# Kernel tuning notes

Measured on AMD Instinct MI355X. Metric: run time of the kernel, lower is better.

Reference implementation:

```python
import jax, jax.numpy as jnp
import numpy as np

S = 3136        # tokens (56x56 patch grid, single image segment -> full attention)
H = 16          # num_heads
D = 80          # head_dim (= head_dim_ori = PADDING_HEAD_DIM)
HID = H * D     # 1280
SCALE = 1.0 / float(np.sqrt(D))  # qkScale = 1/sqrt(head_dim_ori)


def _rope_tables(s, d, base=10000.0):
    # rotate_half style: cos/sin of shape [s, d], duplicated over the two halves
    half = d // 2
    inv_freq = 1.0 / (base ** (np.arange(0, half, dtype=np.float32) / half))
    freqs = np.outer(np.arange(s, dtype=np.float32), inv_freq)  # [s, d/2]
    emb = np.concatenate([freqs, freqs], axis=-1)               # [s, d]
    return jnp.asarray(np.cos(emb)), jnp.asarray(np.sin(emb))


def setup_inputs() -> dict:
    key = jax.random.key(0)
    ks = jax.random.split(key, 6)
    cos, sin = _rope_tables(S, D)
    return {
        "hidden_states": jax.random.normal(ks[0], (S, HID), jnp.float32),
        "x_norm": jax.random.normal(ks[1], (S, HID), jnp.float32),
        "qkv_w": jax.random.normal(ks[2], (3 * HID, HID), jnp.float32) * 0.02,
        "qkv_b": jax.random.normal(ks[3], (3 * HID,), jnp.float32) * 0.02,
        "proj_w": jax.random.normal(ks[4], (HID, HID), jnp.float32) * 0.02,
        "proj_b": jax.random.normal(ks[5], (HID,), jnp.float32) * 0.02,
        "cos": cos,
        "sin": sin,
    }


def _rotate_half(x):
    x1, x2 = jnp.split(x, 2, axis=-1)
    return jnp.concatenate([-x2, x1], axis=-1)


def reference(hidden_states, x_norm, qkv_w, qkv_b, proj_w, proj_b, cos, sin):
    # fused QKV linear (transposeB=True) + split into q,k,v along last dim
    qkv = x_norm @ qkv_w.T + qkv_b                      # [S, 3*HID]
    q, k, v = jnp.split(qkv, 3, axis=-1)                # each [S, HID]
    q = q.reshape(S, H, D)
    k = k.reshape(S, H, D)
    v = v.reshape(S, H, D)
    # inline RoPE on q and k (rotate_half over full head_dim)
    c = cos[:, None, :]; s = sin[:, None, :]           # [S,1,D]
    q = q * c + _rotate_half(q) * s
    k = k * c + _rotate_half(k) * s
    # full self-attention (PA_ENCODER, single segment = seq_len S)
    scores = jnp.einsum('shd,thd->hst', q, k) * SCALE   # [H,S,S]
    probs = jax.nn.softmax(scores, axis=-1)
    attn = jnp.einsum('hst,thd->shd', probs, v)         # [S,H,D]
    attn = attn.reshape(S, HID)
    # output projection + residual add
    out = attn @ proj_w.T + proj_b
    return hidden_states + out
```

## Files before the change

### kernel.cpp

```cpp
#include <hip/hip_runtime.h>
#include <hip/hip_bf16.h>

#define S_   3136
#define H_   16
#define D_   80
#define DP_  96
#define HID_ 1280

typedef short  bf16x8 __attribute__((ext_vector_type(8)));
typedef short  bf16x4 __attribute__((ext_vector_type(4)));
typedef float  f32x4  __attribute__((ext_vector_type(4)));

__device__ __forceinline__ float b2f(unsigned short u) {
    union { unsigned int i; float f; } c;
    c.i = ((unsigned int)u) << 16;
    return c.f;
}
__device__ __forceinline__ unsigned short f2b(float f) {
    union { unsigned int i; float f; } c;
    c.f = f;
    unsigned int x = c.i;
    unsigned int lsb = (x >> 16) & 1u;
    x += 0x7fffu + lsb;
    return (unsigned short)(x >> 16);
}

#define N4_X 1003520
#define N4_Q 1228800
#define N4_P 409600

__global__ __launch_bounds__(256)
void cast3_kernel(const float* __restrict__ x0, unsigned short* __restrict__ y0,
                  const float* __restrict__ x1, unsigned short* __restrict__ y1,
                  const float* __restrict__ x2, unsigned short* __restrict__ y2)
{
    int i = blockIdx.x * 256 + threadIdx.x;
    const float* src; unsigned short* dst;
    if (i < N4_X)               { src = x0; dst = y0; }
    else if (i < N4_X + N4_Q)   { src = x1; dst = y1; i -= N4_X; }
    else if (i < N4_X + N4_Q + N4_P) { src = x2; dst = y2; i -= N4_X + N4_Q; }
    else return;
    float4 v = ((const float4*)src)[i];
    ushort4 o;
    o.x = f2b(v.x); o.y = f2b(v.y); o.z = f2b(v.z); o.w = f2b(v.w);
    ((ushort4*)dst)[i] = o;
}

#define ASTR 40

__global__ __launch_bounds__(256)
void qkv_mfma_kernel(const unsigned short* __restrict__ Ab,
                     const unsigned short* __restrict__ Wb,
                     const float* __restrict__ bias,
                     unsigned short* __restrict__ qo, unsigned short* __restrict__ ko,
                     unsigned short* __restrict__ vtb)
{
    __shared__ __align__(16) short As[2][128][ASTR];
    __shared__ __align__(16) short Bs[2][128][ASTR];
    int m0 = blockIdx.x * 128;
    int n0 = blockIdx.y * 128;
    int t = threadIdx.x;
    int wave = t >> 6, lane = t & 63, lq = lane & 15, quad = lane >> 4;
    int wr = wave >> 1, wc = wave & 1;

    int r0  = t >> 2;
    int r1  = r0 + 64;
    int kc0 = (t & 3) << 3;
    const unsigned short* pa0 = Ab + (size_t)min(m0 + r0, S_ - 1) * HID_ + kc0;
    const unsigned short* pa1 = Ab + (size_t)min(m0 + r1, S_ - 1) * HID_ + kc0;
    const unsigned short* pb0 = Wb + (size_t)(n0 + r0) * HID_ + kc0;
    const unsigned short* pb1 = Wb + (size_t)(n0 + r1) * HID_ + kc0;

    const bf16x8* afp[2][4]; const bf16x8* bfp[2][4];
    #pragma unroll
    for (int s = 0; s < 2; ++s)
        #pragma unroll
        for (int i = 0; i < 4; ++i) {
            afp[s][i] = (const bf16x8*)&As[s][wr * 64 + i * 16 + lq][quad * 8];
            bfp[s][i] = (const bf16x8*)&Bs[s][wc * 64 + i * 16 + lq][quad * 8];
        }

    f32x4 acc[4][4];
    #pragma unroll
    for (int i = 0; i < 4; ++i)
        #pragma unroll
        for (int j = 0; j < 4; ++j) acc[i][j] = (f32x4){0.f, 0.f, 0.f, 0.f};

    bf16x8 va[2][2], vb[2][2];
    #pragma unroll
    for (int s = 0; s < 2; ++s) {
        va[s][0] = *(const bf16x8*)(pa0 + s * 32);
        va[s][1] = *(const bf16x8*)(pa1 + s * 32);
        vb[s][0] = *(const bf16x8*)(pb0 + s * 32);
        vb[s][1] = *(const bf16x8*)(pb1 + s * 32);
    }

    for (int kt = 0; kt < HID_; kt += 64) {
        __syncthreads();
        #pragma unroll
        for (int s = 0; s < 2; ++s) {
            *(bf16x8*)&As[s][r0][kc0] = va[s][0];
            *(bf16x8*)&As[s][r1][kc0] = va[s][1];
            *(bf16x8*)&Bs[s][r0][kc0] = vb[s][0];
            *(bf16x8*)&Bs[s][r1][kc0] = vb[s][1];
        }
        __syncthreads();
        if (kt + 64 < HID_) {
            #pragma unroll
            for (int s = 0; s < 2; ++s) {
                va[s][0] = *(const bf16x8*)(pa0 + kt + 64 + s * 32);
                va[s][1] = *(const bf16x8*)(pa1 + kt + 64 + s * 32);
                vb[s][0] = *(const bf16x8*)(pb0 + kt + 64 + s * 32);
                vb[s][1] = *(const bf16x8*)(pb1 + kt + 64 + s * 32);
            }
        }
        #pragma unroll
        for (int s = 0; s < 2; ++s) {
            bf16x8 af[4], bfr[4];
            #pragma unroll
            for (int i = 0; i < 4; ++i) af[i]  = *afp[s][i];
            #pragma unroll
            for (int j = 0; j < 4; ++j) bfr[j] = *bfp[s][j];
            #pragma unroll
            for (int i = 0; i < 4; ++i)
                #pragma unroll
                for (int j = 0; j < 4; ++j)
                    acc[i][j] = __builtin_amdgcn_mfma_f32_16x16x32_bf16(af[i], bfr[j], acc[i][j], 0, 0, 0);
        }
    }

    #pragma unroll
    for (int i = 0; i < 4; ++i)
        #pragma unroll
        for (int j = 0; j < 4; ++j)
            #pragma unroll
            for (int reg = 0; reg < 4; ++reg) {
                int row = m0 + wr * 64 + i * 16 + quad * 4 + reg;
                if (row >= S_) continue;
                int col = n0 + wc * 64 + j * 16 + lq;
                float val = acc[i][j][reg] + bias[col];
                int which = col / HID_;
                int rem   = col - which * HID_;
                int h     = rem / D_;
                int d     = rem - h * D_;
                if (which == 0)      qo[((size_t)h * S_ + row) * D_ + d] = f2b(val);
                else if (which == 1) ko[((size_t)h * S_ + row) * D_ + d] = f2b(val);
                else                 vtb[((size_t)h * D_ + d) * S_ + row] = f2b(val);
            }
}

__global__ __launch_bounds__(256)
void proj_mfma_kernel(const unsigned short* __restrict__ Ab,
                      const unsigned short* __restrict__ Wb,
                      const float* __restrict__ bias, const float* __restrict__ hidden,
                      float* __restrict__ out)
{
    __shared__ __align__(16) short As[64][ASTR];
    __shared__ __align__(16) short Bs[64][ASTR];
    int m0 = blockIdx.x * 64;
    int n0 = blockIdx.y * 64;
    int t = threadIdx.x;
    int wave = t >> 6, lane = t & 63, lq = lane & 15, quad = lane >> 4;
    int wr = wave >> 1, wc = wave & 1;

    int r  = t >> 2;
    int kc0 = (t & 3) << 3;
    const unsigned short* pa = Ab + (size_t)(m0 + r) * HID_ + kc0;
    const unsigned short* pb = Wb + (size_t)(n0 + r) * HID_ + kc0;
    short* sa = &As[r][kc0];
    short* sb = &Bs[r][kc0];

    const bf16x8* afp[2]; const bf16x8* bfp[2];
    #pragma unroll
    for (int i = 0; i < 2; ++i) {
        afp[i] = (const bf16x8*)&As[wr * 32 + i * 16 + lq][quad * 8];
        bfp[i] = (const bf16x8*)&Bs[wc * 32 + i * 16 + lq][quad * 8];
    }

    f32x4 acc[2][2];
    #pragma unroll
    for (int i = 0; i < 2; ++i)
        #pragma unroll
        for (int j = 0; j < 2; ++j) acc[i][j] = (f32x4){0.f, 0.f, 0.f, 0.f};

    bf16x8 va = *(const bf16x8*)(pa);
    bf16x8 vb = *(const bf16x8*)(pb);

    for (int kt = 0; kt < HID_; kt += 32) {
        __syncthreads();
        *(bf16x8*)sa = va;
        *(bf16x8*)sb = vb;
        __syncthreads();
        if (kt + 32 < HID_) {
            va = *(const bf16x8*)(pa + kt + 32);
            vb = *(const bf16x8*)(pb + kt + 32);
        }
        bf16x8 af[2], bfr[2];
        #pragma unroll
        for (int i = 0; i < 2; ++i) af[i]  = *afp[i];
        #pragma unroll
        for (int j = 0; j < 2; ++j) bfr[j] = *bfp[j];
        #pragma unroll
        for (int i = 0; i < 2; ++i)
            #pragma unroll
            for (int j = 0; j < 2; ++j)
                acc[i][j] = __builtin_amdgcn_mfma_f32_16x16x32_bf16(af[i], bfr[j], acc[i][j], 0, 0, 0);
    }

    #pragma unroll
    for (int i = 0; i < 2; ++i)
        #pragma unroll
        for (int j = 0; j < 2; ++j)
            #pragma unroll
            for (int reg = 0; reg < 4; ++reg) {
                int row = m0 + wr * 32 + i * 16 + quad * 4 + reg;
                int col = n0 + wc * 32 + j * 16 + lq;
                out[(size_t)row * HID_ + col] =
                    acc[i][j][reg] + bias[col] + hidden[(size_t)row * HID_ + col];
            }
}

__global__ void rope_kernel(const unsigned short* __restrict__ q, const unsigned short* __restrict__ k,
                            const float* __restrict__ cost, const float* __restrict__ sint,
                            unsigned short* __restrict__ qb, unsigned short* __restrict__ kb)
{
    const float QSCALE = 0.11180339887498949f * 1.4426950408889634f;
    int idx = blockIdx.x * 256 + threadIdx.x;
    const int total = H_ * S_ * 40;
    if (idx >= total) return;
    int d  = idx % 40;
    int hs = idx / 40;
    int s  = hs % S_;
    size_t base  = (size_t)hs * D_;
    size_t base9 = (size_t)hs * DP_;
    float c1 = cost[s * D_ + d];
    float s1 = sint[s * D_ + d];
    float c2 = cost[s * D_ + d + 40];
    float s2 = sint[s * D_ + d + 40];
    float x1 = b2f(q[base + d]), x2 = b2f(q[base + d + 40]);
    qb[base9 + d]      = f2b((x1 * c1 - x2 * s1) * QSCALE);
    qb[base9 + d + 40] = f2b((x2 * c2 + x1 * s2) * QSCALE);
    x1 = b2f(k[base + d]); x2 = b2f(k[base + d + 40]);
    kb[base9 + d]      = f2b(x1 * c1 - x2 * s1);
    kb[base9 + d + 40] = f2b(x2 * c2 + x1 * s2);
    if (d < 16) {
        qb[base9 + 80 + d] = 0;
        kb[base9 + 80 + d] = 0;
    }
}

#define KSTRIDE 104
#define VSTRIDE 72
#define PSTRIDE 68

__global__ __launch_bounds__(256)
void attn_kernel(const unsigned short* __restrict__ Qb,
                 const unsigned short* __restrict__ Kb,
                 const unsigned short* __restrict__ Vtb,
                 unsigned short* __restrict__ attnb)
{
    __shared__ __align__(16) short Ks[64][KSTRIDE];
    __shared__ __align__(16) short Vs[96][VSTRIDE];
    __shared__ __align__(16) short Ps[4][16][PSTRIDE];

    int h   = blockIdx.y;
    int qb0 = blockIdx.x * 64;
    int t    = threadIdx.x;
    int wave = t >> 6;
    int lane = t & 63;
    int lq   = lane & 15;
    int quad = lane >> 4;

    const unsigned short* Qrow = Qb + ((size_t)h * S_ + qb0 + wave * 16 + lq) * DP_;
    bf16x8 qf[3];
    #pragma unroll
    for (int kc = 0; kc < 3; ++kc)
        qf[kc] = *(const bf16x8*)(Qrow + kc * 32 + quad * 8);

    f32x4 O[5];
    #pragma unroll
    for (int dt = 0; dt < 5; ++dt) O[dt] = (f32x4){0.f, 0.f, 0.f, 0.f};
    float l_acc[4] = {0.f, 0.f, 0.f, 0.f};

    int srow = t & 63;
    int w    = t >> 6;
    int vr0  = t >> 3;
    int vc   = (t & 7) << 3;
    const unsigned short* Kg = Kb  + (size_t)h * S_ * DP_ + (size_t)srow * DP_;
    const unsigned short* Vg = Vtb + (size_t)h * D_ * S_;
    short* kl0 = &Ks[srow][(w    ) * 8];
    short* kl1 = &Ks[srow][(w + 4) * 8];
    short* kl2 = &Ks[srow][(w + 8) * 8];

    const int NKB = S_ / 64;
    bf16x8 pk0, pk1, pk2, pv0, pv1, pv2;
    {
        pk0 = *(const bf16x8*)(Kg + (w    ) * 8);
        pk1 = *(const bf16x8*)(Kg + (w + 4) * 8);
        pk2 = *(const bf16x8*)(Kg + (w + 8) * 8);
        const unsigned short* vg = Vg + vc;
        pv0 = *(const bf16x8*)(vg + (size_t)(vr0     ) * S_);
        pv1 = *(const bf16x8*)(vg + (size_t)(vr0 + 32) * S_);
        pv2 = *(const bf16x8*)(vg + (size_t)(vr0 + 64) * S_);
    }

    for (int kb = 0; kb < NKB; ++kb) {
        __syncthreads();
        *(bf16x8*)kl0 = pk0;
        *(bf16x8*)kl1 = pk1;
        *(bf16x8*)kl2 = pk2;
        *(bf16x8*)&Vs[vr0     ][vc] = pv0;
        *(bf16x8*)&Vs[vr0 + 32][vc] = pv1;
        *(bf16x8*)&Vs[vr0 + 64][vc] = pv2;
        __syncthreads();

        if (kb + 1 < NKB) {
            const unsigned short* kg = Kg + (size_t)(kb + 1) * 64 * DP_;
            pk0 = *(const bf16x8*)(kg + (w    ) * 8);
            pk1 = *(const bf16x8*)(kg + (w + 4) * 8);
            pk2 = *(const bf16x8*)(kg + (w + 8) * 8);
            const unsigned short* vg = Vg + (kb + 1) * 64 + vc;
            pv0 = *(const bf16x8*)(vg + (size_t)(vr0     ) * S_);
            pv1 = *(const bf16x8*)(vg + (size_t)(vr0 + 32) * S_);
            pv2 = *(const bf16x8*)(vg + (size_t)(vr0 + 64) * S_);
        }

        f32x4 sc[4];
        #pragma unroll
        for (int nt = 0; nt < 4; ++nt) {
            sc[nt] = (f32x4){0.f, 0.f, 0.f, 0.f};
            #pragma unroll
            for (int kc = 0; kc < 3; ++kc) {
                bf16x8 kf = *(const bf16x8*)&Ks[nt * 16 + lq][kc * 32 + quad * 8];
                sc[nt] = __builtin_amdgcn_mfma_f32_16x16x32_bf16(qf[kc], kf, sc[nt], 0, 0, 0);
            }
        }

        #pragma unroll
        for (int reg = 0; reg < 4; ++reg) {
            float p0 = exp2f(sc[0][reg]);
            float p1 = exp2f(sc[1][reg]);
            float p2 = exp2f(sc[2][reg]);
            float p3 = exp2f(sc[3][reg]);
            l_acc[reg] += (p0 + p1) + (p2 + p3);
            int prow = quad * 4 + reg;
            Ps[wave][prow][ 0 + lq] = (short)(__float_as_uint(p0) >> 16);
            Ps[wave][prow][16 + lq] = (short)(__float_as_uint(p1) >> 16);
            Ps[wave][prow][32 + lq] = (short)(__float_as_uint(p2) >> 16);
            Ps[wave][prow][48 + lq] = (short)(__float_as_uint(p3) >> 16);
        }

        #pragma unroll
        for (int kc = 0; kc < 2; ++kc) {
            union { bf16x8 v8; bf16x4 v4[2]; } pf;
            pf.v4[0] = *(const bf16x4*)&Ps[wave][lq][kc * 32 + quad * 8];
            pf.v4[1] = *(const bf16x4*)&Ps[wave][lq][kc * 32 + quad * 8 + 4];
            #pragma unroll
            for (int dt = 0; dt < 5; ++dt) {
                bf16x8 vf = *(const bf16x8*)&Vs[dt * 16 + lq][kc * 32 + quad * 8];
                O[dt] = __builtin_amdgcn_mfma_f32_16x16x32_bf16(pf.v8, vf, O[dt], 0, 0, 0);
            }
        }
    }

    #pragma unroll
    for (int reg = 0; reg < 4; ++reg) {
        float l = l_acc[reg];
        #pragma unroll
        for (int off = 1; off < 16; off <<= 1)
            l += __shfl_xor(l, off, 16);
        float linv = 1.0f / l;
        int s = qb0 + wave * 16 + quad * 4 + reg;
        unsigned short* orow = attnb + (size_t)s * HID_ + h * D_;
        #pragma unroll
        for (int dt = 0; dt < 5; ++dt)
            orow[dt * 16 + lq] = f2b(O[dt][reg] * linv);
    }
}

extern "C" void kernel_launch(void* const* d_in, const int* in_sizes, int n_in,
                              void* d_out, int out_size, void* d_ws, size_t ws_size,
                              hipStream_t stream)
{
    const float* hidden = (const float*)d_in[0];
    const float* x_norm = (const float*)d_in[1];
    const float* qkv_w  = (const float*)d_in[2];
    const float* qkv_b  = (const float*)d_in[3];
    const float* proj_w = (const float*)d_in[4];
    const float* proj_b = (const float*)d_in[5];
    const float* cost   = (const float*)d_in[6];
    const float* sint   = (const float*)d_in[7];
    float* out = (float*)d_out;

    unsigned short* w      = (unsigned short*)d_ws;
    unsigned short* qbuf   = w;
    unsigned short* kbuf   = qbuf + 4014080;
    unsigned short* vtb    = kbuf + 4014080;
    unsigned short* kbb    = vtb + 4064256;
    unsigned short* xb     = kbb + 4816896;
    unsigned short* wqkvb  = xb + 4014080;
    unsigned short* wprojb = wqkvb + 4915200;
    unsigned short* qbb    = wqkvb;
    unsigned short* abuf   = qbuf;

    cast3_kernel<<<(N4_X + N4_Q + N4_P + 255) / 256, 256, 0, stream>>>(
        x_norm, xb, qkv_w, wqkvb, proj_w, wprojb);

    qkv_mfma_kernel<<<dim3(25, 30), 256, 0, stream>>>(xb, wqkvb, qkv_b, qbuf, kbuf, vtb);
    rope_kernel<<<(H_ * S_ * 40 + 255) / 256, 256, 0, stream>>>(qbuf, kbuf, cost, sint, qbb, kbb);
    attn_kernel<<<dim3(S_ / 64, H_), 256, 0, stream>>>(qbb, kbb, vtb, abuf);
    proj_mfma_kernel<<<dim3(49, 20), 256, 0, stream>>>(abuf, wprojb, proj_b, hidden, out);
}
```

Measured before the change: 347.3 us.

## Keep attention probabilities in registers via transposed QK^T MFMA, dropping LDS P round-trip

Swaps the MFMA operand order for the score product so each lane holds scores for a single query row across several keys. The bf16 probabilities can then be packed with v_cvt_pk_bf16_f32 directly into the A operand of the PV MFMA, which removes the per-wave Ps shared-memory buffer and its scatter stores and reloads. The V tile is shrunk to 80 rows, skipping the padding loads, and the row-sum reduction is simplified to a single accumulator with fewer shuffles. V is now read from LDS with a permuted k-index split into two 4-element loads per fragment, so the result depends on that permutation exactly matching the new P layout, and the conversion uses round-to-nearest rather than truncation.

```diff
diff --git a/kernel.cpp b/kernel.cpp
--- a/kernel.cpp
+++ b/kernel.cpp
@@ -23,6 +23,11 @@
     unsigned int lsb = (x >> 16) & 1u;
     x += 0x7fffu + lsb;
     return (unsigned short)(x >> 16);
+}
+__device__ __forceinline__ unsigned int cvt_pk_bf16(float lo, float hi) {
+    unsigned int r;
+    asm("v_cvt_pk_bf16_f32 %0, %1, %2" : "=v"(r) : "v"(lo), "v"(hi));
+    return r;
 }
 
 #define N4_X 1003520
@@ -251,7 +256,6 @@
 
 #define KSTRIDE 104
 #define VSTRIDE 72
-#define PSTRIDE 68
 
 __global__ __launch_bounds__(256)
 void attn_kernel(const unsigned short* __restrict__ Qb,
@@ -260,8 +264,7 @@
                  unsigned short* __restrict__ attnb)
 {
     __shared__ __align__(16) short Ks[64][KSTRIDE];
-    __shared__ __align__(16) short Vs[96][VSTRIDE];
-    __shared__ __align__(16) short Ps[4][16][PSTRIDE];
+    __shared__ __align__(16) short Vs[80][VSTRIDE];
 
     int h   = blockIdx.y;
     int qb0 = blockIdx.x * 64;
@@ -280,7 +283,7 @@
     f32x4 O[5];
     #pragma unroll
     for (int dt = 0; dt < 5; ++dt) O[dt] = (f32x4){0.f, 0.f, 0.f, 0.f};
-    float l_acc[4] = {0.f, 0.f, 0.f, 0.f};
+    float l_acc = 0.f;
 
     int srow = t & 63;
     int w    = t >> 6;
@@ -301,7 +304,7 @@
         const unsigned short* vg = Vg + vc;
         pv0 = *(const bf16x8*)(vg + (size_t)(vr0     ) * S_);
         pv1 = *(const bf16x8*)(vg + (size_t)(vr0 + 32) * S_);
-        pv2 = *(const bf16x8*)(vg + (size_t)(vr0 + 64) * S_);
+        if (vr0 < 16) pv2 = *(const bf16x8*)(vg + (size_t)(vr0 + 64) * S_);
     }
 
     for (int kb = 0; kb < NKB; ++kb) {
@@ -311,7 +314,7 @@
         *(bf16x8*)kl2 = pk2;
         *(bf16x8*)&Vs[vr0     ][vc] = pv0;
         *(bf16x8*)&Vs[vr0 + 32][vc] = pv1;
-        *(bf16x8*)&Vs[vr0 + 64][vc] = pv2;
+        if (vr0 < 16) *(bf16x8*)&Vs[vr0 + 64][vc] = pv2;
         __syncthreads();
 
         if (kb + 1 < NKB) {
@@ -322,7 +325,7 @@
             const unsigned short* vg = Vg + (kb + 1) * 64 + vc;
             pv0 = *(const bf16x8*)(vg + (size_t)(vr0     ) * S_);
             pv1 = *(const bf16x8*)(vg + (size_t)(vr0 + 32) * S_);
-            pv2 = *(const bf16x8*)(vg + (size_t)(vr0 + 64) * S_);
+            if (vr0 < 16) pv2 = *(const bf16x8*)(vg + (size_t)(vr0 + 64) * S_);
         }
 
         f32x4 sc[4];
@@ -332,43 +335,49 @@
             #pragma unroll
             for (int kc = 0; kc < 3; ++kc) {
                 bf16x8 kf = *(const bf16x8*)&Ks[nt * 16 + lq][kc * 32 + quad * 8];
-                sc[nt] = __builtin_amdgcn_mfma_f32_16x16x32_bf16(qf[kc], kf, sc[nt], 0, 0, 0);
+                sc[nt] = __builtin_amdgcn_mfma_f32_16x16x32_bf16(kf, qf[kc], sc[nt], 0, 0, 0);
             }
         }
 
-        #pragma unroll
-        for (int reg = 0; reg < 4; ++reg) {
-            float p0 = exp2f(sc[0][reg]);
-            float p1 = exp2f(sc[1][reg]);
-            float p2 = exp2f(sc[2][reg]);
-            float p3 = exp2f(sc[3][reg]);
-            l_acc[reg] += (p0 + p1) + (p2 + p3);
-            int prow = quad * 4 + reg;
-            Ps[wave][prow][ 0 + lq] = (short)(__float_as_uint(p0) >> 16);
-            Ps[wave][prow][16 + lq] = (short)(__float_as_uint(p1) >> 16);
-            Ps[wave][prow][32 + lq] = (short)(__float_as_uint(p2) >> 16);
-            Ps[wave][prow][48 + lq] = (short)(__float_as_uint(p3) >> 16);
-        }
-
+        float p[4][4];
+        #pragma unroll
+        for (int nt = 0; nt < 4; ++nt)
+            #pragma unroll
+            for (int r = 0; r < 4; ++r)
+                p[nt][r] = exp2f(sc[nt][r]);
+
+        l_acc += ((p[0][0] + p[0][1]) + (p[0][2] + p[0][3]))
+               + ((p[1][0] + p[1][1]) + (p[1][2] + p[1][3]))
+               + ((p[2][0] + p[2][1]) + (p[2][2] + p[2][3]))
+               + ((p[3][0] + p[3][1]) + (p[3][2] + p[3][3]));
+
+        union { bf16x8 v8; unsigned int d[4]; } pa[2];
         #pragma unroll
         for (int kc = 0; kc < 2; ++kc) {
-            union { bf16x8 v8; bf16x4 v4[2]; } pf;
-            pf.v4[0] = *(const bf16x4*)&Ps[wave][lq][kc * 32 + quad * 8];
-            pf.v4[1] = *(const bf16x4*)&Ps[wave][lq][kc * 32 + quad * 8 + 4];
+            pa[kc].d[0] = cvt_pk_bf16(p[2 * kc    ][0], p[2 * kc    ][1]);
+            pa[kc].d[1] = cvt_pk_bf16(p[2 * kc    ][2], p[2 * kc    ][3]);
+            pa[kc].d[2] = cvt_pk_bf16(p[2 * kc + 1][0], p[2 * kc + 1][1]);
+            pa[kc].d[3] = cvt_pk_bf16(p[2 * kc + 1][2], p[2 * kc + 1][3]);
+        }
+
+        #pragma unroll
+        for (int kc = 0; kc < 2; ++kc) {
             #pragma unroll
             for (int dt = 0; dt < 5; ++dt) {
-                bf16x8 vf = *(const bf16x8*)&Vs[dt * 16 + lq][kc * 32 + quad * 8];
-                O[dt] = __builtin_amdgcn_mfma_f32_16x16x32_bf16(pf.v8, vf, O[dt], 0, 0, 0);
+                union { bf16x8 v8; bf16x4 v4[2]; } vv;
+                vv.v4[0] = *(const bf16x4*)&Vs[dt * 16 + lq][kc * 32 +      quad * 4];
+                vv.v4[1] = *(const bf16x4*)&Vs[dt * 16 + lq][kc * 32 + 16 + quad * 4];
+                O[dt] = __builtin_amdgcn_mfma_f32_16x16x32_bf16(pa[kc].v8, vv.v8, O[dt], 0, 0, 0);
             }
         }
     }
 
+    float lf = l_acc;
+    lf += __shfl_xor(lf, 16);
+    lf += __shfl_xor(lf, 32);
     #pragma unroll
     for (int reg = 0; reg < 4; ++reg) {
-        float l = l_acc[reg];
-        #pragma unroll
-        for (int off = 1; off < 16; off <<= 1)
-            l += __shfl_xor(l, off, 16);
+        float l = __shfl(lf, quad * 4 + reg, 16);
         float linv = 1.0f / l;
         int s = qb0 + wave * 16 + quad * 4 + reg;
         unsigned short* orow = attnb + (size_t)s * HID_ + h * D_;
```

After: 338.2 us. -2.6%, faster.
